# Kernel optimization log

Measured on AMD Instinct MI355X. Metric: run time of the kernel, lower is better.

Reference implementation:

```python
import jax, jax.numpy as jnp
import numpy as np

IMG_C = 256
GC = 32  # graph_channel; must equal graph feature dim 32 for the residual


def setup_inputs() -> dict:
    key = jax.random.key(0)
    ks = jax.random.split(key, 10)
    B, N, WH_SIDE = 8, 4096, 64
    s = lambda fan_in: 1.0 / np.sqrt(fan_in)
    return {
        "input_graph": jax.random.normal(ks[0], (B, N, GC), jnp.float32),
        "input_image": jax.random.normal(ks[1], (B, IMG_C, WH_SIDE, WH_SIDE), jnp.float32),
        # Conv1d(kernel=1) weights stored as [out, in]
        "Wq": jax.random.uniform(ks[2], (GC, 32), jnp.float32, -s(32), s(32)),
        "bq": jax.random.uniform(ks[3], (GC,), jnp.float32, -s(32), s(32)),
        "Wk": jax.random.uniform(ks[4], (GC, IMG_C), jnp.float32, -s(IMG_C), s(IMG_C)),
        "bk": jax.random.uniform(ks[5], (GC,), jnp.float32, -s(IMG_C), s(IMG_C)),
        "Wv": jax.random.uniform(ks[6], (GC, IMG_C), jnp.float32, -s(IMG_C), s(IMG_C)),
        "bv": jax.random.uniform(ks[7], (GC,), jnp.float32, -s(IMG_C), s(IMG_C)),
        "Wc": jax.random.uniform(ks[8], (GC, GC), jnp.float32, -s(GC), s(GC)),
        "bc": jax.random.uniform(ks[9], (GC,), jnp.float32, -s(GC), s(GC)),
    }


def reference(input_graph, input_image, Wq, bq, Wk, bk, Wv, bv, Wc, bc):
    B, C, W, H = input_image.shape
    img = input_image.reshape(B, C, W * H)                      # [B, C, L]
    # 1x1 conv projections == channel matmuls
    K = jnp.einsum('oc,bcl->bol', Wk, img) + bk[None, :, None]  # [B, GC, L]
    V = jnp.einsum('oc,bcl->bol', Wv, img) + bv[None, :, None]  # [B, GC, L]
    # Q: graph [B, N, 32] -> conv over channel dim -> [B, N, GC]
    Q = jnp.einsum('oc,bnc->bno', Wq, input_graph) + bq[None, None, :]
    att = jnp.einsum('bno,bol->bnl', Q, K) / jnp.sqrt(jnp.float32(GC))  # [B, N, L]
    # NOTE: original softmax is over dim=1 (the node/query axis)
    att = jax.nn.softmax(att, axis=1)
    message = jnp.einsum('bol,bnl->bon', V, att)                # [B, GC, N]
    out = input_graph.transpose(0, 2, 1) + (
        jnp.einsum('oc,bcn->bon', Wc, message) + bc[None, :, None]
    )                                                           # [B, GC, N]
    return out.transpose(0, 2, 1)                               # [B, N, GC]
```

## Files before the change

kernel.cpp:

```cpp
#include <hip/hip_runtime.h>

#define BB 8
#define NN 4096
#define LL 4096
#define CC 256

typedef short bf16x8 __attribute__((ext_vector_type(8)));
typedef _Float16 f16x8 __attribute__((ext_vector_type(8)));
typedef __fp16 hf16x2 __attribute__((ext_vector_type(2)));
typedef float f32x4 __attribute__((ext_vector_type(4)));

__device__ __forceinline__ short f2bf(float f) {
  union { float f; unsigned u; } v; v.f = f;
  unsigned r = v.u + 0x7fffu + ((v.u >> 16) & 1u);
  return (short)(r >> 16);
}
__device__ __forceinline__ bf16x8 ld8(const float* __restrict__ fp) {
  float4 a = *(const float4*)fp;
  float4 b = *(const float4*)(fp + 4);
  bf16x8 r;
  r[0] = f2bf(a.x); r[1] = f2bf(a.y); r[2] = f2bf(a.z); r[3] = f2bf(a.w);
  r[4] = f2bf(b.x); r[5] = f2bf(b.y); r[6] = f2bf(b.z); r[7] = f2bf(b.w);
  return r;
}

__global__ __launch_bounds__(256) void ka_proj(
    const float* __restrict__ graph, const float* __restrict__ img,
    const float* __restrict__ Wq, const float* __restrict__ bq,
    const float* __restrict__ Wk, const float* __restrict__ bk,
    const float* __restrict__ Wv, const float* __restrict__ bv,
    short* __restrict__ Qb, short* __restrict__ Kt, _Float16* __restrict__ Vt,
    float* __restrict__ Zbuf)
{
  const int tid = threadIdx.x;
  const int w = tid >> 6, lane = tid & 63, lo = lane & 15, q = lane >> 4;
  const int bid = blockIdx.x;
  if (bid < 512) {
    const int b = bid >> 6;
    if (tid < 64) Zbuf[(size_t)b * LL + ((bid & 63) << 6) + tid] = 0.0f;
    const int lt = ((bid & 63) << 6) + (w << 4);
    f32x4 aK0 = {0,0,0,0}, aK1 = {0,0,0,0}, aV0 = {0,0,0,0}, aV1 = {0,0,0,0};
    const float* ib = img + (size_t)b * CC * LL + lt + lo;
    #pragma unroll
    for (int cs = 0; cs < 8; ++cs) {
      const int c0 = cs * 32 + q * 8;
      bf16x8 bi;
      #pragma unroll
      for (int j = 0; j < 8; ++j) bi[j] = f2bf(ib[(size_t)(c0 + j) * LL]);
      bf16x8 wk0 = ld8(Wk + lo * CC + c0);
      bf16x8 wk1 = ld8(Wk + (lo + 16) * CC + c0);
      bf16x8 wv0 = ld8(Wv + lo * CC + c0);
      bf16x8 wv1 = ld8(Wv + (lo + 16) * CC + c0);
      aK0 = __builtin_amdgcn_mfma_f32_16x16x32_bf16(wk0, bi, aK0, 0, 0, 0);
      aK1 = __builtin_amdgcn_mfma_f32_16x16x32_bf16(wk1, bi, aK1, 0, 0, 0);
      aV0 = __builtin_amdgcn_mfma_f32_16x16x32_bf16(wv0, bi, aV0, 0, 0, 0);
      aV1 = __builtin_amdgcn_mfma_f32_16x16x32_bf16(wv1, bi, aV1, 0, 0, 0);
    }
    const float kscale = 0.2550348663f;
    const size_t row = ((size_t)b * LL + lt + lo) * 32;
    short4 s0, s1;
    s0.x = f2bf((aK0[0] + bk[q * 4 + 0]) * kscale);
    s0.y = f2bf((aK0[1] + bk[q * 4 + 1]) * kscale);
    s0.z = f2bf((aK0[2] + bk[q * 4 + 2]) * kscale);
    s0.w = f2bf((aK0[3] + bk[q * 4 + 3]) * kscale);
    s1.x = f2bf((aK1[0] + bk[16 + q * 4 + 0]) * kscale);
    s1.y = f2bf((aK1[1] + bk[16 + q * 4 + 1]) * kscale);
    s1.z = f2bf((aK1[2] + bk[16 + q * 4 + 2]) * kscale);
    s1.w = f2bf((aK1[3] + bk[16 + q * 4 + 3]) * kscale);
    *(short4*)(Kt + row + q * 4) = s0;
    *(short4*)(Kt + row + 16 + q * 4) = s1;
    union { hf16x2 h[2]; uint2 u; } p0, p1;
    p0.h[0] = __builtin_amdgcn_cvt_pkrtz(aV0[0] + bv[q * 4 + 0], aV0[1] + bv[q * 4 + 1]);
    p0.h[1] = __builtin_amdgcn_cvt_pkrtz(aV0[2] + bv[q * 4 + 2], aV0[3] + bv[q * 4 + 3]);
    p1.h[0] = __builtin_amdgcn_cvt_pkrtz(aV1[0] + bv[16 + q * 4 + 0], aV1[1] + bv[16 + q * 4 + 1]);
    p1.h[1] = __builtin_amdgcn_cvt_pkrtz(aV1[2] + bv[16 + q * 4 + 2], aV1[3] + bv[16 + q * 4 + 3]);
    *(uint2*)(Vt + row + q * 4) = p0.u;
    *(uint2*)(Vt + row + 16 + q * 4) = p1.u;
  } else {
    const int t = bid - 512;
    const int b = t >> 6;
    const int nt = ((t & 63) << 6) + (w << 4);
    bf16x8 ag = ld8(graph + ((size_t)b * NN + nt + lo) * 32 + q * 8);
    bf16x8 w0 = ld8(Wq + lo * 32 + q * 8);
    bf16x8 w1 = ld8(Wq + (lo + 16) * 32 + q * 8);
    f32x4 z = {0,0,0,0};
    f32x4 a0 = __builtin_amdgcn_mfma_f32_16x16x32_bf16(ag, w0, z, 0, 0, 0);
    f32x4 a1 = __builtin_amdgcn_mfma_f32_16x16x32_bf16(ag, w1, z, 0, 0, 0);
    const float b0 = bq[lo], b1 = bq[lo + 16];
    #pragma unroll
    for (int r = 0; r < 4; ++r) {
      const size_t rowq = ((size_t)b * NN + nt + q * 4 + r) * 32;
      Qb[rowq + lo] = f2bf(a0[r] + b0);
      Qb[rowq + 16 + lo] = f2bf(a1[r] + b1);
    }
  }
}

__global__ __launch_bounds__(256, 8) void kb1_z(
    const short* __restrict__ Qb, const short* __restrict__ Kt,
    float* __restrict__ Z)
{
  const int tid = threadIdx.x;
  const int w = tid >> 6, lane = tid & 63, lo = lane & 15, q = lane >> 4;
  const int bid = blockIdx.x;
  const int b = bid >> 8;
  const int l0 = ((bid >> 2) & 63) << 6;
  const int nq = bid & 3;
  bf16x8 kf[4];
  #pragma unroll
  for (int f = 0; f < 4; ++f)
    kf[f] = *(const bf16x8*)(Kt + ((size_t)b * LL + l0 + f * 16 + lo) * 32 + q * 8);
  float za[4][4] = {{0}};
  const short* qbase = Qb + ((size_t)b * NN + nq * 1024 + w * 256 + lo) * 32 + q * 8;
  bf16x8 qf = *(const bf16x8*)qbase;
  for (int it = 0; it < 16; ++it) {
    const int itn = (it + 1 < 16) ? it + 1 : it;
    bf16x8 qn = *(const bf16x8*)(qbase + itn * 512);
    #pragma unroll
    for (int f = 0; f < 4; ++f) {
      f32x4 z = {0,0,0,0};
      f32x4 c = __builtin_amdgcn_mfma_f32_16x16x32_bf16(kf[f], qf, z, 0, 0, 0);
      #pragma unroll
      for (int r = 0; r < 4; ++r) za[f][r] += __builtin_amdgcn_exp2f(c[r]);
    }
    qf = qn;
  }
  #pragma unroll
  for (int m = 1; m < 16; m <<= 1)
    #pragma unroll
    for (int f = 0; f < 4; ++f)
      #pragma unroll
      for (int r = 0; r < 4; ++r)
        za[f][r] += __shfl_xor(za[f][r], m, 64);
  if (lo == 0) {
    #pragma unroll
    for (int f = 0; f < 4; ++f)
      #pragma unroll
      for (int r = 0; r < 4; ++r)
        atomicAdd(&Z[(size_t)b * LL + l0 + f * 16 + q * 4 + r], za[f][r]);
  }
}

__global__ __launch_bounds__(256) void kb2_scale(
    const _Float16* __restrict__ Vt, const float* __restrict__ Z,
    _Float16* __restrict__ Vpp)
{
  const int tid = threadIdx.x;
  const int b = blockIdx.x >> 6;
  const int l = ((blockIdx.x & 63) << 6) + (tid & 63);
  const int og = tid >> 6;
  const float inv = __builtin_amdgcn_rcpf(Z[(size_t)b * LL + l]) * 4096.0f;
  const f16x8 vv = *(const f16x8*)(Vt + ((size_t)b * LL + l) * 32 + og * 8);
  #pragma unroll
  for (int j = 0; j < 8; ++j)
    Vpp[((size_t)b * 32 + og * 8 + j) * LL + l] = (_Float16)((float)vv[j] * inv);
}

__global__ __launch_bounds__(256, 8) void kc1_attn(
    const short* __restrict__ Qb, const short* __restrict__ Kt,
    const _Float16* __restrict__ Vpp, float* __restrict__ msgpart)
{
  __shared__ __align__(16) unsigned char smem[18432];
  const int tid = threadIdx.x;
  const int w = tid >> 6, lane = tid & 63, lo = lane & 15, q = lane >> 4;
  const int bid = blockIdx.x;
  const int b = bid >> 8;
  const int half = (bid >> 7) & 1;
  const int n0 = (bid & 127) << 5;
  _Float16* Pw = (_Float16*)smem + w * (32 * 72);
  float* MS = (float*)smem;
  const bf16x8 qf0 = *(const bf16x8*)(Qb + ((size_t)b * NN + n0 + lo) * 32 + q * 8);
  const bf16x8 qf1 = *(const bf16x8*)(Qb + ((size_t)b * NN + n0 + 16 + lo) * 32 + q * 8);
  f32x4 m00 = {0,0,0,0}, m01 = {0,0,0,0}, m10 = {0,0,0,0}, m11 = {0,0,0,0};
  const short* ktb = Kt + (size_t)b * LL * 32 + lo * 32 + q * 8;
  const _Float16* vb0 = Vpp + ((size_t)b * 32 + lo) * LL;
  const _Float16* vb1 = vb0 + (size_t)16 * LL;
  const int lc0 = half * 32 + w * 8;
  bf16x8 kfN[4];
  #pragma unroll
  for (int f = 0; f < 4; ++f)
    kfN[f] = *(const bf16x8*)(ktb + (size_t)(lc0 * 64 + f * 16) * 32);
  for (int lc = lc0; lc < lc0 + 8; ++lc) {
    const int lbase = lc * 64;
    bf16x8 kfC[4];
    #pragma unroll
    for (int f = 0; f < 4; ++f) kfC[f] = kfN[f];
    f16x8 vA0 = *(const f16x8*)(vb0 + lbase + q * 8);
    f16x8 vA1 = *(const f16x8*)(vb0 + lbase + 32 + q * 8);
    f16x8 vB0 = *(const f16x8*)(vb1 + lbase + q * 8);
    f16x8 vB1 = *(const f16x8*)(vb1 + lbase + 32 + q * 8);
    const int lcn = (lc + 1 < lc0 + 8) ? lc + 1 : lc;
    #pragma unroll
    for (int f = 0; f < 4; ++f)
      kfN[f] = *(const bf16x8*)(ktb + (size_t)(lcn * 64 + f * 16) * 32);
    #pragma unroll
    for (int f = 0; f < 4; ++f) {
      f32x4 z = {0,0,0,0};
      f32x4 c0 = __builtin_amdgcn_mfma_f32_16x16x32_bf16(kfC[f], qf0, z, 0, 0, 0);
      f32x4 c1 = __builtin_amdgcn_mfma_f32_16x16x32_bf16(kfC[f], qf1, z, 0, 0, 0);
      union { hf16x2 h[2]; uint2 u; } pk0, pk1;
      pk0.h[0] = __builtin_amdgcn_cvt_pkrtz(__builtin_amdgcn_exp2f(c0[0]),
                                            __builtin_amdgcn_exp2f(c0[1]));
      pk0.h[1] = __builtin_amdgcn_cvt_pkrtz(__builtin_amdgcn_exp2f(c0[2]),
                                            __builtin_amdgcn_exp2f(c0[3]));
      pk1.h[0] = __builtin_amdgcn_cvt_pkrtz(__builtin_amdgcn_exp2f(c1[0]),
                                            __builtin_amdgcn_exp2f(c1[1]));
      pk1.h[1] = __builtin_amdgcn_cvt_pkrtz(__builtin_amdgcn_exp2f(c1[2]),
                                            __builtin_amdgcn_exp2f(c1[3]));
      *(uint2*)&Pw[lo * 72 + f * 16 + q * 4] = pk0.u;
      *(uint2*)&Pw[(16 + lo) * 72 + f * 16 + q * 4] = pk1.u;
    }
    {
      f16x8 pa00 = *(const f16x8*)&Pw[lo * 72 + q * 8];
      f16x8 pa01 = *(const f16x8*)&Pw[lo * 72 + 32 + q * 8];
      f16x8 pa10 = *(const f16x8*)&Pw[(16 + lo) * 72 + q * 8];
      f16x8 pa11 = *(const f16x8*)&Pw[(16 + lo) * 72 + 32 + q * 8];
      m00 = __builtin_amdgcn_mfma_f32_16x16x32_f16(pa00, vA0, m00, 0, 0, 0);
      m10 = __builtin_amdgcn_mfma_f32_16x16x32_f16(pa10, vA0, m10, 0, 0, 0);
      m01 = __builtin_amdgcn_mfma_f32_16x16x32_f16(pa00, vB0, m01, 0, 0, 0);
      m11 = __builtin_amdgcn_mfma_f32_16x16x32_f16(pa10, vB0, m11, 0, 0, 0);
      m00 = __builtin_amdgcn_mfma_f32_16x16x32_f16(pa01, vA1, m00, 0, 0, 0);
      m10 = __builtin_amdgcn_mfma_f32_16x16x32_f16(pa11, vA1, m10, 0, 0, 0);
      m01 = __builtin_amdgcn_mfma_f32_16x16x32_f16(pa01, vB1, m01, 0, 0, 0);
      m11 = __builtin_amdgcn_mfma_f32_16x16x32_f16(pa11, vB1, m11, 0, 0, 0);
    }
  }
  float* MSw = MS + w * (32 * 36);
  #pragma unroll
  for (int r = 0; r < 4; ++r) {
    MSw[(q * 4 + r) * 36 + lo] = m00[r];
    MSw[(q * 4 + r) * 36 + 16 + lo] = m01[r];
    MSw[(16 + q * 4 + r) * 36 + lo] = m10[r];
    MSw[(16 + q * 4 + r) * 36 + 16 + lo] = m11[r];
  }
  __syncthreads();
  const int nl = tid >> 3, oq = (tid & 7) << 2;
  f32x4 s = *(const f32x4*)&MS[0 * 1152 + nl * 36 + oq];
  s += *(const f32x4*)&MS[1 * 1152 + nl * 36 + oq];
  s += *(const f32x4*)&MS[2 * 1152 + nl * 36 + oq];
  s += *(const f32x4*)&MS[3 * 1152 + nl * 36 + oq];
  *(f32x4*)(msgpart + (((size_t)half * BB + b) * NN + n0 + nl) * 32 + oq) = s;
}

__global__ __launch_bounds__(256) void kc2_out(
    const float* __restrict__ msgpart, const float* __restrict__ graph,
    const float* __restrict__ Wc, const float* __restrict__ bc,
    float* __restrict__ out)
{
  const int tid = threadIdx.x;
  const int b = blockIdx.x >> 7;
  const int n = ((blockIdx.x & 127) << 5) + (tid >> 3);
  const int oq = (tid & 7) << 2;
  const float* mp0 = msgpart + ((size_t)b * NN + n) * 32;
  const float* mp1 = msgpart + ((size_t)(BB + b) * NN + n) * 32;
  float m[32];
  #pragma unroll
  for (int c4 = 0; c4 < 8; ++c4) {
    f32x4 a = *(const f32x4*)(mp0 + c4 * 4);
    f32x4 bsum = *(const f32x4*)(mp1 + c4 * 4);
    f32x4 s = a + bsum;
    m[c4 * 4 + 0] = s[0]; m[c4 * 4 + 1] = s[1];
    m[c4 * 4 + 2] = s[2]; m[c4 * 4 + 3] = s[3];
  }
  #pragma unroll
  for (int j = 0; j < 4; ++j) {
    const int o = oq + j;
    float acc = 0.0f;
    #pragma unroll
    for (int c4 = 0; c4 < 8; ++c4) {
      f32x4 wv = *(const f32x4*)(Wc + o * 32 + c4 * 4);
      acc += wv[0] * m[c4 * 4 + 0] + wv[1] * m[c4 * 4 + 1]
           + wv[2] * m[c4 * 4 + 2] + wv[3] * m[c4 * 4 + 3];
    }
    const size_t idx = ((size_t)b * NN + n) * 32 + o;
    out[idx] = acc * (1.0f / 4096.0f) + bc[o] + graph[idx];
  }
}

extern "C" void kernel_launch(void* const* d_in, const int* in_sizes, int n_in,
                              void* d_out, int out_size, void* d_ws, size_t ws_size,
                              hipStream_t stream) {
  const float* graph = (const float*)d_in[0];
  const float* img   = (const float*)d_in[1];
  const float* Wq    = (const float*)d_in[2];
  const float* bq    = (const float*)d_in[3];
  const float* Wk    = (const float*)d_in[4];
  const float* bk    = (const float*)d_in[5];
  const float* Wv    = (const float*)d_in[6];
  const float* bv    = (const float*)d_in[7];
  const float* Wc    = (const float*)d_in[8];
  const float* bc    = (const float*)d_in[9];
  char* ws = (char*)d_ws;
  short*    Qb  = (short*)(ws + 0);
  short*    Kt  = (short*)(ws + 2097152);
  _Float16* Vt  = (_Float16*)(ws + 4194304);
  _Float16* Vpp = (_Float16*)(ws + 6291456);
  float*    Zb  = (float*)(ws + 8388608);
  float*    Mp  = (float*)(ws + 8519680);
  ka_proj<<<dim3(1024), dim3(256), 0, stream>>>(graph, img, Wq, bq, Wk, bk, Wv, bv,
                                                Qb, Kt, Vt, Zb);
  kb1_z<<<dim3(2048), dim3(256), 0, stream>>>(Qb, Kt, Zb);
  kb2_scale<<<dim3(512), dim3(256), 0, stream>>>(Vt, Zb, Vpp);
  kc1_attn<<<dim3(2048), dim3(256), 0, stream>>>(Qb, Kt, Vpp, Mp);
  kc2_out<<<dim3(1024), dim3(256), 0, stream>>>(Mp, graph, Wc, bc, (float*)d_out);
}
```

Measured before the change: 196.0 us.

## Software-pipeline attention with double-buffered P tiles and split Z-sum chains

The attention kernel now double-buffers the per-wave P tile in shared memory. It computes the next chunk's QK^T and exp into one buffer while the current chunk's PV MFMAs read the other, so exp/convert work overlaps matrix ops. The Z kernel processes two query streams per iteration with separate accumulators, giving more independent MFMA/exp chains. This doubles shared memory and register use and lowers the occupancy hints (8→4 and 8→6), which may reduce latency hiding.

```diff
diff --git a/kernel.cpp b/kernel.cpp
--- a/kernel.cpp
+++ b/kernel.cpp
@@ -96,7 +96,7 @@
   }
 }
 
-__global__ __launch_bounds__(256, 8) void kb1_z(
+__global__ __launch_bounds__(256, 6) void kb1_z(
     const short* __restrict__ Qb, const short* __restrict__ Kt,
     float* __restrict__ Z)
 {
@@ -110,21 +110,33 @@
   #pragma unroll
   for (int f = 0; f < 4; ++f)
     kf[f] = *(const bf16x8*)(Kt + ((size_t)b * LL + l0 + f * 16 + lo) * 32 + q * 8);
-  float za[4][4] = {{0}};
+  float za[4][4] = {{0}}, zb[4][4] = {{0}};
   const short* qbase = Qb + ((size_t)b * NN + nq * 1024 + w * 256 + lo) * 32 + q * 8;
-  bf16x8 qf = *(const bf16x8*)qbase;
-  for (int it = 0; it < 16; ++it) {
-    const int itn = (it + 1 < 16) ? it + 1 : it;
-    bf16x8 qn = *(const bf16x8*)(qbase + itn * 512);
+  bf16x8 qa = *(const bf16x8*)qbase;
+  bf16x8 qb = *(const bf16x8*)(qbase + 8 * 512);
+  #pragma unroll
+  for (int it = 0; it < 8; ++it) {
+    const int itn = (it + 1 < 8) ? it + 1 : it;
+    bf16x8 qan = *(const bf16x8*)(qbase + itn * 512);
+    bf16x8 qbn = *(const bf16x8*)(qbase + (8 + itn) * 512);
     #pragma unroll
     for (int f = 0; f < 4; ++f) {
       f32x4 z = {0,0,0,0};
-      f32x4 c = __builtin_amdgcn_mfma_f32_16x16x32_bf16(kf[f], qf, z, 0, 0, 0);
+      f32x4 ca = __builtin_amdgcn_mfma_f32_16x16x32_bf16(kf[f], qa, z, 0, 0, 0);
+      f32x4 cb = __builtin_amdgcn_mfma_f32_16x16x32_bf16(kf[f], qb, z, 0, 0, 0);
       #pragma unroll
-      for (int r = 0; r < 4; ++r) za[f][r] += __builtin_amdgcn_exp2f(c[r]);
+      for (int r = 0; r < 4; ++r) {
+        za[f][r] += __builtin_amdgcn_exp2f(ca[r]);
+        zb[f][r] += __builtin_amdgcn_exp2f(cb[r]);
+      }
     }
-    qf = qn;
-  }
+    qa = qan; qb = qbn;
+  }
+  #pragma unroll
+  for (int f = 0; f < 4; ++f)
+    #pragma unroll
+    for (int r = 0; r < 4; ++r)
+      za[f][r] += zb[f][r];
   #pragma unroll
   for (int m = 1; m < 16; m <<= 1)
     #pragma unroll
@@ -156,19 +168,54 @@
     Vpp[((size_t)b * 32 + og * 8 + j) * LL + l] = (_Float16)((float)vv[j] * inv);
 }
 
-__global__ __launch_bounds__(256, 8) void kc1_attn(
+__device__ __forceinline__ void load_kf(bf16x8 kf[4], const short* __restrict__ ktb,
+                                        int lc) {
+  #pragma unroll
+  for (int f = 0; f < 4; ++f)
+    kf[f] = *(const bf16x8*)(ktb + (size_t)(lc * 64 + f * 16) * 32);
+}
+__device__ __forceinline__ void load_v(f16x8 v[4], const _Float16* __restrict__ vb0,
+                                       const _Float16* __restrict__ vb1, int lc, int q) {
+  const int lbase = lc * 64;
+  v[0] = *(const f16x8*)(vb0 + lbase + q * 8);
+  v[1] = *(const f16x8*)(vb0 + lbase + 32 + q * 8);
+  v[2] = *(const f16x8*)(vb1 + lbase + q * 8);
+  v[3] = *(const f16x8*)(vb1 + lbase + 32 + q * 8);
+}
+__device__ __forceinline__ void compute_P(const bf16x8 kf[4], bf16x8 qf0, bf16x8 qf1,
+                                          _Float16* __restrict__ Pb, int lo, int q) {
+  #pragma unroll
+  for (int f = 0; f < 4; ++f) {
+    f32x4 z = {0,0,0,0};
+    f32x4 c0 = __builtin_amdgcn_mfma_f32_16x16x32_bf16(kf[f], qf0, z, 0, 0, 0);
+    f32x4 c1 = __builtin_amdgcn_mfma_f32_16x16x32_bf16(kf[f], qf1, z, 0, 0, 0);
+    union { hf16x2 h[2]; uint2 u; } pk0, pk1;
+    pk0.h[0] = __builtin_amdgcn_cvt_pkrtz(__builtin_amdgcn_exp2f(c0[0]),
+                                          __builtin_amdgcn_exp2f(c0[1]));
+    pk0.h[1] = __builtin_amdgcn_cvt_pkrtz(__builtin_amdgcn_exp2f(c0[2]),
+                                          __builtin_amdgcn_exp2f(c0[3]));
+    pk1.h[0] = __builtin_amdgcn_cvt_pkrtz(__builtin_amdgcn_exp2f(c1[0]),
+                                          __builtin_amdgcn_exp2f(c1[1]));
+    pk1.h[1] = __builtin_amdgcn_cvt_pkrtz(__builtin_amdgcn_exp2f(c1[2]),
+                                          __builtin_amdgcn_exp2f(c1[3]));
+    *(uint2*)&Pb[lo * 72 + f * 16 + q * 4] = pk0.u;
+    *(uint2*)&Pb[(16 + lo) * 72 + f * 16 + q * 4] = pk1.u;
+  }
+}
+
+__global__ __launch_bounds__(256, 4) void kc1_attn(
     const short* __restrict__ Qb, const short* __restrict__ Kt,
     const _Float16* __restrict__ Vpp, float* __restrict__ msgpart)
 {
-  __shared__ __align__(16) unsigned char smem[18432];
+  __shared__ __align__(16) unsigned char smem[36864];
   const int tid = threadIdx.x;
   const int w = tid >> 6, lane = tid & 63, lo = lane & 15, q = lane >> 4;
   const int bid = blockIdx.x;
   const int b = bid >> 8;
   const int half = (bid >> 7) & 1;
   const int n0 = (bid & 127) << 5;
-  _Float16* Pw = (_Float16*)smem + w * (32 * 72);
-  float* MS = (float*)smem;
+  _Float16* const Pb0 = (_Float16*)(smem + w * 9216);
+  _Float16* const Pb1 = Pb0 + 32 * 72;
   const bf16x8 qf0 = *(const bf16x8*)(Qb + ((size_t)b * NN + n0 + lo) * 32 + q * 8);
   const bf16x8 qf1 = *(const bf16x8*)(Qb + ((size_t)b * NN + n0 + 16 + lo) * 32 + q * 8);
   f32x4 m00 = {0,0,0,0}, m01 = {0,0,0,0}, m10 = {0,0,0,0}, m11 = {0,0,0,0};
@@ -176,56 +223,32 @@
   const _Float16* vb0 = Vpp + ((size_t)b * 32 + lo) * LL;
   const _Float16* vb1 = vb0 + (size_t)16 * LL;
   const int lc0 = half * 32 + w * 8;
-  bf16x8 kfN[4];
-  #pragma unroll
-  for (int f = 0; f < 4; ++f)
-    kfN[f] = *(const bf16x8*)(ktb + (size_t)(lc0 * 64 + f * 16) * 32);
-  for (int lc = lc0; lc < lc0 + 8; ++lc) {
-    const int lbase = lc * 64;
-    bf16x8 kfC[4];
-    #pragma unroll
-    for (int f = 0; f < 4; ++f) kfC[f] = kfN[f];
-    f16x8 vA0 = *(const f16x8*)(vb0 + lbase + q * 8);
-    f16x8 vA1 = *(const f16x8*)(vb0 + lbase + 32 + q * 8);
-    f16x8 vB0 = *(const f16x8*)(vb1 + lbase + q * 8);
-    f16x8 vB1 = *(const f16x8*)(vb1 + lbase + 32 + q * 8);
-    const int lcn = (lc + 1 < lc0 + 8) ? lc + 1 : lc;
-    #pragma unroll
-    for (int f = 0; f < 4; ++f)
-      kfN[f] = *(const bf16x8*)(ktb + (size_t)(lcn * 64 + f * 16) * 32);
-    #pragma unroll
-    for (int f = 0; f < 4; ++f) {
-      f32x4 z = {0,0,0,0};
-      f32x4 c0 = __builtin_amdgcn_mfma_f32_16x16x32_bf16(kfC[f], qf0, z, 0, 0, 0);
-      f32x4 c1 = __builtin_amdgcn_mfma_f32_16x16x32_bf16(kfC[f], qf1, z, 0, 0, 0);
-      union { hf16x2 h[2]; uint2 u; } pk0, pk1;
-      pk0.h[0] = __builtin_amdgcn_cvt_pkrtz(__builtin_amdgcn_exp2f(c0[0]),
-                                            __builtin_amdgcn_exp2f(c0[1]));
-      pk0.h[1] = __builtin_amdgcn_cvt_pkrtz(__builtin_amdgcn_exp2f(c0[2]),
-                                            __builtin_amdgcn_exp2f(c0[3]));
-      pk1.h[0] = __builtin_amdgcn_cvt_pkrtz(__builtin_amdgcn_exp2f(c1[0]),
-                                            __builtin_amdgcn_exp2f(c1[1]));
-      pk1.h[1] = __builtin_amdgcn_cvt_pkrtz(__builtin_amdgcn_exp2f(c1[2]),
-                                            __builtin_amdgcn_exp2f(c1[3]));
-      *(uint2*)&Pw[lo * 72 + f * 16 + q * 4] = pk0.u;
-      *(uint2*)&Pw[(16 + lo) * 72 + f * 16 + q * 4] = pk1.u;
-    }
-    {
-      f16x8 pa00 = *(const f16x8*)&Pw[lo * 72 + q * 8];
-      f16x8 pa01 = *(const f16x8*)&Pw[lo * 72 + 32 + q * 8];
-      f16x8 pa10 = *(const f16x8*)&Pw[(16 + lo) * 72 + q * 8];
-      f16x8 pa11 = *(const f16x8*)&Pw[(16 + lo) * 72 + 32 + q * 8];
-      m00 = __builtin_amdgcn_mfma_f32_16x16x32_f16(pa00, vA0, m00, 0, 0, 0);
-      m10 = __builtin_amdgcn_mfma_f32_16x16x32_f16(pa10, vA0, m10, 0, 0, 0);
-      m01 = __builtin_amdgcn_mfma_f32_16x16x32_f16(pa00, vB0, m01, 0, 0, 0);
-      m11 = __builtin_amdgcn_mfma_f32_16x16x32_f16(pa10, vB0, m11, 0, 0, 0);
-      m00 = __builtin_amdgcn_mfma_f32_16x16x32_f16(pa01, vA1, m00, 0, 0, 0);
-      m10 = __builtin_amdgcn_mfma_f32_16x16x32_f16(pa11, vA1, m10, 0, 0, 0);
-      m01 = __builtin_amdgcn_mfma_f32_16x16x32_f16(pa01, vB1, m01, 0, 0, 0);
-      m11 = __builtin_amdgcn_mfma_f32_16x16x32_f16(pa11, vB1, m11, 0, 0, 0);
-    }
-  }
-  float* MSw = MS + w * (32 * 36);
+  bf16x8 kfs[2][4];
+  load_kf(kfs[0], ktb, lc0);
+  load_kf(kfs[1], ktb, lc0 + 1);
+  compute_P(kfs[0], qf0, qf1, Pb0, lo, q);
+  #pragma unroll
+  for (int i = 0; i < 8; ++i) {
+    _Float16* const bufC = (i & 1) ? Pb1 : Pb0;
+    _Float16* const bufN = (i & 1) ? Pb0 : Pb1;
+    f16x8 pa00 = *(const f16x8*)&bufC[lo * 72 + q * 8];
+    f16x8 pa01 = *(const f16x8*)&bufC[lo * 72 + 32 + q * 8];
+    f16x8 pa10 = *(const f16x8*)&bufC[(16 + lo) * 72 + q * 8];
+    f16x8 pa11 = *(const f16x8*)&bufC[(16 + lo) * 72 + 32 + q * 8];
+    f16x8 vc[4];
+    load_v(vc, vb0, vb1, lc0 + i, q);
+    if (i + 2 <= 7) load_kf(kfs[i & 1], ktb, lc0 + i + 2);
+    if (i + 1 <= 7) compute_P(kfs[1 - (i & 1)], qf0, qf1, bufN, lo, q);
+    m00 = __builtin_amdgcn_mfma_f32_16x16x32_f16(pa00, vc[0], m00, 0, 0, 0);
+    m10 = __builtin_amdgcn_mfma_f32_16x16x32_f16(pa10, vc[0], m10, 0, 0, 0);
+    m01 = __builtin_amdgcn_mfma_f32_16x16x32_f16(pa00, vc[2], m01, 0, 0, 0);
+    m11 = __builtin_amdgcn_mfma_f32_16x16x32_f16(pa10, vc[2], m11, 0, 0, 0);
+    m00 = __builtin_amdgcn_mfma_f32_16x16x32_f16(pa01, vc[1], m00, 0, 0, 0);
+    m10 = __builtin_amdgcn_mfma_f32_16x16x32_f16(pa11, vc[1], m10, 0, 0, 0);
+    m01 = __builtin_amdgcn_mfma_f32_16x16x32_f16(pa01, vc[3], m01, 0, 0, 0);
+    m11 = __builtin_amdgcn_mfma_f32_16x16x32_f16(pa11, vc[3], m11, 0, 0, 0);
+  }
+  float* MSw = (float*)(smem + w * 9216);
   #pragma unroll
   for (int r = 0; r < 4; ++r) {
     MSw[(q * 4 + r) * 36 + lo] = m00[r];
@@ -235,10 +258,10 @@
   }
   __syncthreads();
   const int nl = tid >> 3, oq = (tid & 7) << 2;
-  f32x4 s = *(const f32x4*)&MS[0 * 1152 + nl * 36 + oq];
-  s += *(const f32x4*)&MS[1 * 1152 + nl * 36 + oq];
-  s += *(const f32x4*)&MS[2 * 1152 + nl * 36 + oq];
-  s += *(const f32x4*)&MS[3 * 1152 + nl * 36 + oq];
+  f32x4 s = *(const f32x4*)((float*)(smem + 0 * 9216) + nl * 36 + oq);
+  s += *(const f32x4*)((float*)(smem + 1 * 9216) + nl * 36 + oq);
+  s += *(const f32x4*)((float*)(smem + 2 * 9216) + nl * 36 + oq);
+  s += *(const f32x4*)((float*)(smem + 3 * 9216) + nl * 36 + oq);
   *(f32x4*)(msgpart + (((size_t)half * BB + b) * NN + n0 + nl) * 32 + oq) = s;
 }
 
```

Measured after the change: 225.1 us. +14.9%, slower.

## Feed exp'd scores directly into 16x16x16 MFMA, drop LDS P staging

Applied to the files above, without the earlier changes.

The attention kernel no longer writes the exponentiated score tile to shared memory and reads it back. It uses the 16x16x16 f16 MFMA with V as the A operand, so the score accumulator layout matches the B-operand layout directly and the values stay in registers. This removes the LDS round-trip and its waits, at the cost of dropping the explicit K prefetch and issuing smaller V loads. The Z kernel now preloads all 16 Q fragments and fully unrolls its loop, and both kernels lower their occupancy hint from 8 to 4 blocks, trading occupancy for more registers.

```diff
diff --git a/kernel.cpp b/kernel.cpp
--- a/kernel.cpp
+++ b/kernel.cpp
@@ -7,6 +7,7 @@
 
 typedef short bf16x8 __attribute__((ext_vector_type(8)));
 typedef _Float16 f16x8 __attribute__((ext_vector_type(8)));
+typedef _Float16 f16x4 __attribute__((ext_vector_type(4)));
 typedef __fp16 hf16x2 __attribute__((ext_vector_type(2)));
 typedef float f32x4 __attribute__((ext_vector_type(4)));
 
@@ -96,7 +97,7 @@
   }
 }
 
-__global__ __launch_bounds__(256, 8) void kb1_z(
+__global__ __launch_bounds__(256, 4) void kb1_z(
     const short* __restrict__ Qb, const short* __restrict__ Kt,
     float* __restrict__ Z)
 {
@@ -110,20 +111,21 @@
   #pragma unroll
   for (int f = 0; f < 4; ++f)
     kf[f] = *(const bf16x8*)(Kt + ((size_t)b * LL + l0 + f * 16 + lo) * 32 + q * 8);
+  const short* qbase = Qb + ((size_t)b * NN + nq * 1024 + w * 256 + lo) * 32 + q * 8;
+  bf16x8 qf[16];
+  #pragma unroll
+  for (int it = 0; it < 16; ++it)
+    qf[it] = *(const bf16x8*)(qbase + it * 512);
   float za[4][4] = {{0}};
-  const short* qbase = Qb + ((size_t)b * NN + nq * 1024 + w * 256 + lo) * 32 + q * 8;
-  bf16x8 qf = *(const bf16x8*)qbase;
+  #pragma unroll
   for (int it = 0; it < 16; ++it) {
-    const int itn = (it + 1 < 16) ? it + 1 : it;
-    bf16x8 qn = *(const bf16x8*)(qbase + itn * 512);
     #pragma unroll
     for (int f = 0; f < 4; ++f) {
       f32x4 z = {0,0,0,0};
-      f32x4 c = __builtin_amdgcn_mfma_f32_16x16x32_bf16(kf[f], qf, z, 0, 0, 0);
+      f32x4 c = __builtin_amdgcn_mfma_f32_16x16x32_bf16(kf[f], qf[it], z, 0, 0, 0);
       #pragma unroll
       for (int r = 0; r < 4; ++r) za[f][r] += __builtin_amdgcn_exp2f(c[r]);
     }
-    qf = qn;
   }
   #pragma unroll
   for (int m = 1; m < 16; m <<= 1)
@@ -156,89 +158,61 @@
     Vpp[((size_t)b * 32 + og * 8 + j) * LL + l] = (_Float16)((float)vv[j] * inv);
 }
 
-__global__ __launch_bounds__(256, 8) void kc1_attn(
+__global__ __launch_bounds__(256, 4) void kc1_attn(
     const short* __restrict__ Qb, const short* __restrict__ Kt,
     const _Float16* __restrict__ Vpp, float* __restrict__ msgpart)
 {
-  __shared__ __align__(16) unsigned char smem[18432];
+  __shared__ __align__(16) float MS[4][32 * 36];
   const int tid = threadIdx.x;
   const int w = tid >> 6, lane = tid & 63, lo = lane & 15, q = lane >> 4;
   const int bid = blockIdx.x;
   const int b = bid >> 8;
   const int half = (bid >> 7) & 1;
   const int n0 = (bid & 127) << 5;
-  _Float16* Pw = (_Float16*)smem + w * (32 * 72);
-  float* MS = (float*)smem;
   const bf16x8 qf0 = *(const bf16x8*)(Qb + ((size_t)b * NN + n0 + lo) * 32 + q * 8);
   const bf16x8 qf1 = *(const bf16x8*)(Qb + ((size_t)b * NN + n0 + 16 + lo) * 32 + q * 8);
-  f32x4 m00 = {0,0,0,0}, m01 = {0,0,0,0}, m10 = {0,0,0,0}, m11 = {0,0,0,0};
+  f32x4 mLL = {0,0,0,0}, mHL = {0,0,0,0}, mLH = {0,0,0,0}, mHH = {0,0,0,0};
   const short* ktb = Kt + (size_t)b * LL * 32 + lo * 32 + q * 8;
-  const _Float16* vb0 = Vpp + ((size_t)b * 32 + lo) * LL;
-  const _Float16* vb1 = vb0 + (size_t)16 * LL;
+  const _Float16* vbL = Vpp + ((size_t)b * 32 + lo) * LL;
+  const _Float16* vbH = vbL + (size_t)16 * LL;
   const int lc0 = half * 32 + w * 8;
-  bf16x8 kfN[4];
-  #pragma unroll
-  for (int f = 0; f < 4; ++f)
-    kfN[f] = *(const bf16x8*)(ktb + (size_t)(lc0 * 64 + f * 16) * 32);
   for (int lc = lc0; lc < lc0 + 8; ++lc) {
     const int lbase = lc * 64;
-    bf16x8 kfC[4];
-    #pragma unroll
-    for (int f = 0; f < 4; ++f) kfC[f] = kfN[f];
-    f16x8 vA0 = *(const f16x8*)(vb0 + lbase + q * 8);
-    f16x8 vA1 = *(const f16x8*)(vb0 + lbase + 32 + q * 8);
-    f16x8 vB0 = *(const f16x8*)(vb1 + lbase + q * 8);
-    f16x8 vB1 = *(const f16x8*)(vb1 + lbase + 32 + q * 8);
-    const int lcn = (lc + 1 < lc0 + 8) ? lc + 1 : lc;
-    #pragma unroll
-    for (int f = 0; f < 4; ++f)
-      kfN[f] = *(const bf16x8*)(ktb + (size_t)(lcn * 64 + f * 16) * 32);
     #pragma unroll
     for (int f = 0; f < 4; ++f) {
+      bf16x8 kf = *(const bf16x8*)(ktb + (size_t)(lbase + f * 16) * 32);
+      const int lf = lbase + f * 16 + q * 4;
+      f16x4 vL = *(const f16x4*)(vbL + lf);
+      f16x4 vH = *(const f16x4*)(vbH + lf);
       f32x4 z = {0,0,0,0};
-      f32x4 c0 = __builtin_amdgcn_mfma_f32_16x16x32_bf16(kfC[f], qf0, z, 0, 0, 0);
-      f32x4 c1 = __builtin_amdgcn_mfma_f32_16x16x32_bf16(kfC[f], qf1, z, 0, 0, 0);
-      union { hf16x2 h[2]; uint2 u; } pk0, pk1;
-      pk0.h[0] = __builtin_amdgcn_cvt_pkrtz(__builtin_amdgcn_exp2f(c0[0]),
-                                            __builtin_amdgcn_exp2f(c0[1]));
-      pk0.h[1] = __builtin_amdgcn_cvt_pkrtz(__builtin_amdgcn_exp2f(c0[2]),
-                                            __builtin_amdgcn_exp2f(c0[3]));
-      pk1.h[0] = __builtin_amdgcn_cvt_pkrtz(__builtin_amdgcn_exp2f(c1[0]),
-                                            __builtin_amdgcn_exp2f(c1[1]));
-      pk1.h[1] = __builtin_amdgcn_cvt_pkrtz(__builtin_amdgcn_exp2f(c1[2]),
-                                            __builtin_amdgcn_exp2f(c1[3]));
-      *(uint2*)&Pw[lo * 72 + f * 16 + q * 4] = pk0.u;
-      *(uint2*)&Pw[(16 + lo) * 72 + f * 16 + q * 4] = pk1.u;
-    }
-    {
-      f16x8 pa00 = *(const f16x8*)&Pw[lo * 72 + q * 8];
-      f16x8 pa01 = *(const f16x8*)&Pw[lo * 72 + 32 + q * 8];
-      f16x8 pa10 = *(const f16x8*)&Pw[(16 + lo) * 72 + q * 8];
-      f16x8 pa11 = *(const f16x8*)&Pw[(16 + lo) * 72 + 32 + q * 8];
-      m00 = __builtin_amdgcn_mfma_f32_16x16x32_f16(pa00, vA0, m00, 0, 0, 0);
-      m10 = __builtin_amdgcn_mfma_f32_16x16x32_f16(pa10, vA0, m10, 0, 0, 0);
-      m01 = __builtin_amdgcn_mfma_f32_16x16x32_f16(pa00, vB0, m01, 0, 0, 0);
-      m11 = __builtin_amdgcn_mfma_f32_16x16x32_f16(pa10, vB0, m11, 0, 0, 0);
-      m00 = __builtin_amdgcn_mfma_f32_16x16x32_f16(pa01, vA1, m00, 0, 0, 0);
-      m10 = __builtin_amdgcn_mfma_f32_16x16x32_f16(pa11, vA1, m10, 0, 0, 0);
-      m01 = __builtin_amdgcn_mfma_f32_16x16x32_f16(pa01, vB1, m01, 0, 0, 0);
-      m11 = __builtin_amdgcn_mfma_f32_16x16x32_f16(pa11, vB1, m11, 0, 0, 0);
-    }
-  }
-  float* MSw = MS + w * (32 * 36);
-  #pragma unroll
-  for (int r = 0; r < 4; ++r) {
-    MSw[(q * 4 + r) * 36 + lo] = m00[r];
-    MSw[(q * 4 + r) * 36 + 16 + lo] = m01[r];
-    MSw[(16 + q * 4 + r) * 36 + lo] = m10[r];
-    MSw[(16 + q * 4 + r) * 36 + 16 + lo] = m11[r];
-  }
+      f32x4 c0 = __builtin_amdgcn_mfma_f32_16x16x32_bf16(kf, qf0, z, 0, 0, 0);
+      f32x4 c1 = __builtin_amdgcn_mfma_f32_16x16x32_bf16(kf, qf1, z, 0, 0, 0);
+      union { hf16x2 h[2]; f16x4 v; } p0, p1;
+      p0.h[0] = __builtin_amdgcn_cvt_pkrtz(__builtin_amdgcn_exp2f(c0[0]),
+                                           __builtin_amdgcn_exp2f(c0[1]));
+      p0.h[1] = __builtin_amdgcn_cvt_pkrtz(__builtin_amdgcn_exp2f(c0[2]),
+                                           __builtin_amdgcn_exp2f(c0[3]));
+      p1.h[0] = __builtin_amdgcn_cvt_pkrtz(__builtin_amdgcn_exp2f(c1[0]),
+                                           __builtin_amdgcn_exp2f(c1[1]));
+      p1.h[1] = __builtin_amdgcn_cvt_pkrtz(__builtin_amdgcn_exp2f(c1[2]),
+                                           __builtin_amdgcn_exp2f(c1[3]));
+      mLL = __builtin_amdgcn_mfma_f32_16x16x16f16(vL, p0.v, mLL, 0, 0, 0);
+      mHL = __builtin_amdgcn_mfma_f32_16x16x16f16(vH, p0.v, mHL, 0, 0, 0);
+      mLH = __builtin_amdgcn_mfma_f32_16x16x16f16(vL, p1.v, mLH, 0, 0, 0);
+      mHH = __builtin_amdgcn_mfma_f32_16x16x16f16(vH, p1.v, mHH, 0, 0, 0);
+    }
+  }
+  float* MSw = MS[w];
+  *(f32x4*)&MSw[lo * 36 + q * 4] = mLL;
+  *(f32x4*)&MSw[lo * 36 + 16 + q * 4] = mHL;
+  *(f32x4*)&MSw[(16 + lo) * 36 + q * 4] = mLH;
+  *(f32x4*)&MSw[(16 + lo) * 36 + 16 + q * 4] = mHH;
   __syncthreads();
   const int nl = tid >> 3, oq = (tid & 7) << 2;
-  f32x4 s = *(const f32x4*)&MS[0 * 1152 + nl * 36 + oq];
-  s += *(const f32x4*)&MS[1 * 1152 + nl * 36 + oq];
-  s += *(const f32x4*)&MS[2 * 1152 + nl * 36 + oq];
-  s += *(const f32x4*)&MS[3 * 1152 + nl * 36 + oq];
+  f32x4 s = *(const f32x4*)&MS[0][nl * 36 + oq];
+  s += *(const f32x4*)&MS[1][nl * 36 + oq];
+  s += *(const f32x4*)&MS[2][nl * 36 + oq];
+  s += *(const f32x4*)&MS[3][nl * 36 + oq];
   *(f32x4*)(msgpart + (((size_t)half * BB + b) * NN + n0 + nl) * 32 + oq) = s;
 }
 
```

Result: slower. 217.4 us (+11.0%).
